# Kernel tuning notes

Hardware: AMD Instinct MI355X
Metric: run time of the kernel (lower is better)

The kernel has to match this reference:

```python
import jax, jax.numpy as jnp
import numpy as np

B, T, C = 2, 2048, 2048
N_HEAD = 16
HS = C // N_HEAD
D_LATENT = C // 2


def setup_inputs() -> dict:
    key = jax.random.key(0)
    ks = jax.random.split(key, 7)
    s = 0.02
    return {
        "x": jax.random.normal(ks[0], (B, T, C), dtype=jnp.float32),
        "Wq": jax.random.normal(ks[1], (C, C), dtype=jnp.float32) * s,
        "Wc": jax.random.normal(ks[2], (C, D_LATENT), dtype=jnp.float32) * s,
        "Wk": jax.random.normal(ks[3], (D_LATENT, C), dtype=jnp.float32) * s,
        "Wv": jax.random.normal(ks[4], (D_LATENT, C), dtype=jnp.float32) * s,
        "Wo": jax.random.normal(ks[5], (C, C), dtype=jnp.float32) * s,
        "bo": jnp.zeros((C,), dtype=jnp.float32),
    }


def reference(x, Wq, Wc, Wk, Wv, Wo, bo):
    b, t, c = x.shape
    # projections (torch Linear without bias, weights stored as (in, out))
    q = x @ Wq                    # (B,T,C)
    c_latent = x @ Wc             # (B,T,d_latent)
    k = c_latent @ Wk             # (B,T,C)
    v = c_latent @ Wv             # (B,T,C)
    # split heads -> (B,H,T,hs)
    q = q.reshape(b, t, N_HEAD, HS).transpose(0, 2, 1, 3)
    k = k.reshape(b, t, N_HEAD, HS).transpose(0, 2, 1, 3)
    v = v.reshape(b, t, N_HEAD, HS).transpose(0, 2, 1, 3)
    scale = 1.0 / jnp.sqrt(jnp.asarray(HS, dtype=x.dtype))
    scores = jnp.einsum('bhqd,bhkd->bhqk', q, k) * scale
    causal = jnp.tril(jnp.ones((t, t), dtype=bool))
    scores = jnp.where(causal, scores, jnp.finfo(scores.dtype).min)
    attn = jax.nn.softmax(scores, axis=-1)
    y = jnp.einsum('bhqk,bhkd->bhqd', attn, v)      # (B,H,T,hs)
    y = y.transpose(0, 2, 1, 3).reshape(b, t, c)
    return y @ Wo + bo
```

## Files before the change

### kernel.cpp

```cpp
#include <hip/hip_runtime.h>
#include <hip/hip_bf16.h>
#include <math.h>

typedef __hip_bfloat16 bf16;
typedef __attribute__((ext_vector_type(8))) short bf16x8;
typedef __attribute__((ext_vector_type(4))) float f32x4;

#define B_  2
#define T_  2048
#define C_  2048
#define H_  16
#define HS_ 128
#define DL_ 1024
#define M_  (B_ * T_)
#define NT64_ 32

__device__ inline void lds16(const bf16* g, bf16* l) {
    __builtin_amdgcn_global_load_lds(
        (const __attribute__((address_space(1))) void*)g,
        (__attribute__((address_space(3))) void*)l, 16, 0, 0);
}

__global__ __launch_bounds__(256) void cast_bf16_k(
    const float* __restrict__ in, bf16* __restrict__ out)
{
    const size_t i = ((size_t)blockIdx.x * 256 + threadIdx.x) * 8;
    const float4 a = *(const float4*)(in + i);
    const float4 b = *(const float4*)(in + i + 4);
    bf16 o[8];
    o[0] = __float2bfloat16(a.x); o[1] = __float2bfloat16(a.y);
    o[2] = __float2bfloat16(a.z); o[3] = __float2bfloat16(a.w);
    o[4] = __float2bfloat16(b.x); o[5] = __float2bfloat16(b.y);
    o[6] = __float2bfloat16(b.z); o[7] = __float2bfloat16(b.w);
    *(uint4*)(out + i) = *(const uint4*)o;
}

__global__ __launch_bounds__(256) void transpose_cast5(
    const float* __restrict__ s0, const float* __restrict__ s1,
    const float* __restrict__ s2, const float* __restrict__ s3,
    const float* __restrict__ s4,
    bf16* __restrict__ d0, bf16* __restrict__ d1, bf16* __restrict__ d2,
    bf16* __restrict__ d3, bf16* __restrict__ d4)
{
    const float* in; bf16* out; int R, Cc;
    switch (blockIdx.z) {
        case 0: in = s0; out = d0; R = C_;  Cc = C_;  break;
        case 1: in = s1; out = d1; R = C_;  Cc = DL_; break;
        case 2: in = s2; out = d2; R = DL_; Cc = C_;  break;
        case 3: in = s3; out = d3; R = DL_; Cc = C_;  break;
        default: in = s4; out = d4; R = C_; Cc = C_;  break;
    }
    const int bx = blockIdx.x * 32, by = blockIdx.y * 32;
    if (bx >= Cc || by >= R) return;
    __shared__ float t[32][33];
    const int tx = threadIdx.x & 31, ty = threadIdx.x >> 5;
#pragma unroll
    for (int i = 0; i < 32; i += 8)
        t[ty + i][tx] = in[(size_t)(by + ty + i) * Cc + bx + tx];
    __syncthreads();
#pragma unroll
    for (int i = 0; i < 32; i += 8)
        out[(size_t)(bx + ty + i) * R + by + tx] = __float2bfloat16(t[tx][ty + i]);
}

#define GEMM250_CORE(A_, Bt_, ldA_, ldB_, Kdim_)                               \
    __shared__ __align__(16) bf16 smem[3 * 24576];                 \
    const int tid  = threadIdx.x;                                              \
    const int lane = tid & 63;                                                 \
    const int wid  = tid >> 6;                                       \
    const int wr   = wid >> 1, wc = wid & 1;                    \
    const int quad = lane >> 4, l16 = lane & 15;                               \
    const int sw8  = (l16 >> 1) & 7;                                           \
    f32x4 acc[4][4];                                                           \
    _Pragma("unroll")                                                          \
    for (int i = 0; i < 4; i++)                                                \
        _Pragma("unroll")                                                      \
        for (int j = 0; j < 4; j++) acc[i][j] = (f32x4){0.f, 0.f, 0.f, 0.f};   \
    const int sr  = tid >> 3;                                       \
    const int ssl = ((tid & 7) ^ ((sr >> 1) & 7)) * 8;                         \
    const bf16* pa = (A_)  + (size_t)(m0 + sr) * (ldA_) + ssl;                 \
    const bf16* pb = (Bt_) + (size_t)(n0 + sr) * (ldB_) + ssl;                 \
    const size_t a64 = (size_t)64 * (ldA_), b64 = (size_t)64 * (ldB_);         \
    const int NT = (Kdim_) / 64;                                               \
    _Pragma("unroll")                                                          \
    for (int pt = 0; pt < 2; ++pt) {                  \
        bf16* dst = smem + pt * 24576 + tid * 8;                               \
        const size_t ko = (size_t)pt * 64;                                     \
        lds16(pa + ko,           dst);                                         \
        lds16(pa + a64 + ko,     dst + 4096);                                  \
        lds16(pa + 2*a64 + ko,   dst + 8192);                                  \
        lds16(pa + 3*a64 + ko,   dst + 12288);                                 \
        lds16(pb + ko,           dst + 16384);                                 \
        lds16(pb + b64 + ko,     dst + 20480);                                 \
    }                                                                          \
    int cur = 0, nxt2 = 2;                                                     \
    for (int t = 0; t < NT; ++t) {                                             \
        if (t == NT - 1) {                                                     \
            __asm__ __volatile__("s_waitcnt vmcnt(0)" ::: "memory");           \
        } else {                                                               \
            __asm__ __volatile__("s_waitcnt vmcnt(6)" ::: "memory");           \
        }                                                                      \
        __builtin_amdgcn_s_barrier();                                          \
        __builtin_amdgcn_sched_barrier(0);                                     \
        if (t + 2 < NT) {                                                      \
            bf16* dst = smem + nxt2 * 24576 + tid * 8;                         \
            const size_t ko = (size_t)(t + 2) * 64;                            \
            lds16(pa + ko,           dst);                                     \
            lds16(pa + a64 + ko,     dst + 4096);                              \
            lds16(pa + 2*a64 + ko,   dst + 8192);                              \
            lds16(pa + 3*a64 + ko,   dst + 12288);                             \
            lds16(pb + ko,           dst + 16384);                             \
            lds16(pb + b64 + ko,     dst + 20480);                             \
        }                                                                      \
        const bf16* Ab = smem + cur * 24576;                                   \
        const bf16* Bb = Ab + 16384;                                           \
        bf16x8 af[4][2], bfr[4][2];                                            \
        _Pragma("unroll")                                                      \
        for (int mi = 0; mi < 4; mi++)                                         \
            _Pragma("unroll")                                                  \
            for (int ks = 0; ks < 2; ks++)                                     \
                af[mi][ks] = *(const bf16x8*)&Ab[(wr*64 + mi*16 + l16)*64 +    \
                                                 (((ks<<2)|quad) ^ sw8)*8];    \
        _Pragma("unroll")                                                      \
        for (int ni = 0; ni < 4; ni++)                                         \
            _Pragma("unroll")                                                  \
            for (int ks = 0; ks < 2; ks++)                                     \
                bfr[ni][ks] = *(const bf16x8*)&Bb[(wc*64 + ni*16 + l16)*64 +   \
                                                  (((ks<<2)|quad) ^ sw8)*8];   \
        __builtin_amdgcn_s_setprio(1);                                         \
        _Pragma("unroll")                                                      \
        for (int ks = 0; ks < 2; ks++)                                         \
            _Pragma("unroll")                                                  \
            for (int mi = 0; mi < 4; mi++)                                     \
                _Pragma("unroll")                                              \
                for (int ni = 0; ni < 4; ni++)                                 \
                    acc[mi][ni] = __builtin_amdgcn_mfma_f32_16x16x32_bf16(     \
                        af[mi][ks], bfr[ni][ks], acc[mi][ni], 0, 0, 0);        \
        __builtin_amdgcn_s_setprio(0);                                         \
        cur  = (cur  == 2) ? 0 : cur  + 1;                                     \
        nxt2 = (nxt2 == 2) ? 0 : nxt2 + 1;                                     \
    }

__global__ __launch_bounds__(512, 2) void gemm_qc_250(
    const bf16* __restrict__ A, const bf16* __restrict__ Bt,
    bf16* __restrict__ Cq, bf16* __restrict__ Cc)
{
    const int m0 = blockIdx.y * 256, n0 = blockIdx.x * 128;
    GEMM250_CORE(A, Bt, C_, C_, C_)
    const bool is_q = (n0 < C_);
    const float scl = is_q ? 0.08838834764831845f : 1.0f;
    bf16* dst = is_q ? Cq : Cc;
    const int ld   = is_q ? C_ : DL_;
    const int coff = is_q ? 0 : C_;
#pragma unroll
    for (int mi = 0; mi < 4; mi++) {
#pragma unroll
        for (int ni = 0; ni < 4; ni++) {
            const int col = n0 - coff + wc * 64 + ni * 16 + l16;
#pragma unroll
            for (int r = 0; r < 4; r++) {
                const int row = m0 + wr * 64 + mi * 16 + quad * 4 + r;
                dst[(size_t)row * ld + col] = __float2bfloat16(acc[mi][ni][r] * scl);
            }
        }
    }
}

__global__ __launch_bounds__(512, 2) void gemm_kv_250(
    const bf16* __restrict__ clat, const bf16* __restrict__ Wk_t,
    const bf16* __restrict__ Wv_t, bf16* __restrict__ kk, bf16* __restrict__ vt)
{
    const int bid = blockIdx.x;
    const bf16 *A, *Bt; bf16* dst; int N, m0, n0;
    if (bid < 256) { A = clat; Bt = Wk_t; dst = kk; N = C_;
                     m0 = (bid >> 4) * 256; n0 = (bid & 15) * 128; }
    else           { const int t2 = bid - 256;
                     A = Wv_t; Bt = clat; dst = vt; N = M_;
                     m0 = (t2 >> 5) * 256; n0 = (t2 & 31) * 128; }
    GEMM250_CORE(A, Bt, DL_, DL_, DL_)
#pragma unroll
    for (int mi = 0; mi < 4; mi++) {
#pragma unroll
        for (int ni = 0; ni < 4; ni++) {
            const int col = n0 + wc * 64 + ni * 16 + l16;
#pragma unroll
            for (int r = 0; r < 4; r++) {
                const int row = m0 + wr * 64 + mi * 16 + quad * 4 + r;
                dst[(size_t)row * N + col] = __float2bfloat16(acc[mi][ni][r]);
            }
        }
    }
}

__global__ __launch_bounds__(512, 2) void gemm_out_250(
    const bf16* __restrict__ A, const bf16* __restrict__ Bt,
    float* __restrict__ Cf32, const float* __restrict__ bias)
{
    const int m0 = blockIdx.y * 256, n0 = blockIdx.x * 128;
    GEMM250_CORE(A, Bt, C_, C_, C_)
#pragma unroll
    for (int mi = 0; mi < 4; mi++) {
#pragma unroll
        for (int ni = 0; ni < 4; ni++) {
            const int col = n0 + wc * 64 + ni * 16 + l16;
#pragma unroll
            for (int r = 0; r < 4; r++) {
                const int row = m0 + wr * 64 + mi * 16 + quad * 4 + r;
                Cf32[(size_t)row * C_ + col] = acc[mi][ni][r] + bias[col];
            }
        }
    }
}

__global__ __launch_bounds__(256, 2) void flash_dual(
    const bf16* __restrict__ Q, const bf16* __restrict__ K,
    const bf16* __restrict__ Vt, bf16* __restrict__ Y)
{
    __shared__ __align__(16) bf16 Ks[2][4][64][32];
    __shared__ __align__(16) bf16 Vs[2][2][128][32];
    __shared__ __align__(16) bf16 Ps[4][16][72];
    const int tid  = threadIdx.x;
    const int lane = tid & 63, wv = tid >> 6;
    const int quad = lane >> 4, l16 = lane & 15;
    const int sw = (l16 >> 1) & 3;
    const int bid = blockIdx.x;
    const int bh = (bid & 7) * 4 + ((bid >> 3) & 3);
    const int pa = bid >> 5;
    const int b = bh >> 4, h = bh & 15;
    const int qA0 = pa * 64, qB0 = (NT64_ - 1 - pa) * 64;
    const int jA = pa + 1;
    const int jB = NT64_ - pa;

    const int sr  = tid >> 2;
    const int ssl = ((tid & 3) ^ ((sr >> 1) & 3)) * 8;

    bf16x8 qfA[4], qfB[4];
    {
        const size_t rA = (size_t)(b * T_ + qA0 + wv * 16 + l16) * C_ + h * HS_;
        const size_t rB = (size_t)(b * T_ + qB0 + wv * 16 + l16) * C_ + h * HS_;
#pragma unroll
        for (int c = 0; c < 4; c++) {
            qfA[c] = *(const bf16x8*)(Q + rA + c * 32 + quad * 8);
            qfB[c] = *(const bf16x8*)(Q + rB + c * 32 + quad * 8);
        }
    }

    f32x4 oA[8], oB[8];
#pragma unroll
    for (int dt = 0; dt < 8; dt++) {
        oA[dt] = (f32x4){0.f, 0.f, 0.f, 0.f};
        oB[dt] = (f32x4){0.f, 0.f, 0.f, 0.f};
    }
    float lA[4] = {0.f, 0.f, 0.f, 0.f}, lB[4] = {0.f, 0.f, 0.f, 0.f};
    const int rbA = qA0 + wv * 16, rbB = qB0 + wv * 16;

    auto stage = [&](int j, int sbuf) {
        const int kv0 = j * 64;
#pragma unroll
        for (int kc = 0; kc < 4; kc++)
            lds16(K + (size_t)(b * T_ + kv0 + sr) * C_ + h * HS_ + kc * 32 + ssl,
                  &Ks[sbuf][kc][0][0] + tid * 8);
#pragma unroll
        for (int vc = 0; vc < 2; vc++)
#pragma unroll
            for (int hf = 0; hf < 2; hf++)
                lds16(Vt + (size_t)(h * HS_ + hf * 64 + sr) * M_ + b * T_ + kv0 + vc * 32 + ssl,
                      &Vs[sbuf][vc][hf * 64][0] + tid * 8);
    };

    auto sm_half = [&](const f32x4* s, int nt0, float* l_s, bool diag,
                       int kv0, int rowbase) {
        float p[2][4];
#pragma unroll
        for (int t = 0; t < 2; t++)
#pragma unroll
            for (int r = 0; r < 4; r++) {
                const int nt = nt0 + t;
                float e = __expf(s[nt][r]);
                if (diag) {
                    const int col = kv0 + nt * 16 + l16;
                    const int row = rowbase + quad * 4 + r;
                    if (col > row) e = 0.f;
                }
                p[t][r] = e;
            }
#pragma unroll
        for (int r = 0; r < 4; r++) l_s[r] += p[0][r] + p[1][r];
#pragma unroll
        for (int t = 0; t < 2; t++)
#pragma unroll
            for (int r = 0; r < 4; r++)
                Ps[wv][quad * 4 + r][(nt0 + t) * 16 + l16] = __float2bfloat16(p[t][r]);
        return *(const bf16x8*)&Ps[wv][l16][nt0 * 16 + quad * 8];
    };

    stage(0, 0);

    for (int j = 0; j < jA; j++) {
        const int kv0 = j * 64;
        stage(j + 1, (j + 1) & 1);
        __asm__ __volatile__("s_waitcnt vmcnt(8)" ::: "memory");
        __builtin_amdgcn_s_barrier();
        const int buf = j & 1;

        f32x4 sA[4], sB[4];
#pragma unroll
        for (int nt = 0; nt < 4; nt++) {
            sA[nt] = (f32x4){0.f, 0.f, 0.f, 0.f};
            sB[nt] = (f32x4){0.f, 0.f, 0.f, 0.f};
        }
        __builtin_amdgcn_s_setprio(1);
#pragma unroll
        for (int c = 0; c < 4; c++) {
            bf16x8 kf[4];
#pragma unroll
            for (int nt = 0; nt < 4; nt++)
                kf[nt] = *(const bf16x8*)&Ks[buf][c][nt * 16 + l16][(quad ^ sw) * 8];
#pragma unroll
            for (int nt = 0; nt < 4; nt++) {
                sB[nt] = __builtin_amdgcn_mfma_f32_16x16x32_bf16(qfB[c], kf[nt], sB[nt], 0, 0, 0);
                sA[nt] = __builtin_amdgcn_mfma_f32_16x16x32_bf16(qfA[c], kf[nt], sA[nt], 0, 0, 0);
            }
        }
        __builtin_amdgcn_s_setprio(0);

        const bool dA = (j == jA - 1);
        const bf16x8 pB0 = sm_half(sB, 0, lB, false, kv0, rbB);
        const bf16x8 pB1 = sm_half(sB, 2, lB, false, kv0, rbB);
        const bf16x8 pA0 = sm_half(sA, 0, lA, dA, kv0, rbA);
        const bf16x8 pA1 = sm_half(sA, 2, lA, dA, kv0, rbA);

        __builtin_amdgcn_s_setprio(1);
#pragma unroll
        for (int dt = 0; dt < 8; dt++) {
            const bf16x8 vf0 = *(const bf16x8*)&Vs[buf][0][dt * 16 + l16][(quad ^ sw) * 8];
            oB[dt] = __builtin_amdgcn_mfma_f32_16x16x32_bf16(pB0, vf0, oB[dt], 0, 0, 0);
            oA[dt] = __builtin_amdgcn_mfma_f32_16x16x32_bf16(pA0, vf0, oA[dt], 0, 0, 0);
        }
#pragma unroll
        for (int dt = 0; dt < 8; dt++) {
            const bf16x8 vf1 = *(const bf16x8*)&Vs[buf][1][dt * 16 + l16][(quad ^ sw) * 8];
            oB[dt] = __builtin_amdgcn_mfma_f32_16x16x32_bf16(pB1, vf1, oB[dt], 0, 0, 0);
            oA[dt] = __builtin_amdgcn_mfma_f32_16x16x32_bf16(pA1, vf1, oA[dt], 0, 0, 0);
        }
        __builtin_amdgcn_s_setprio(0);
        __asm__ __volatile__("s_waitcnt lgkmcnt(0)" ::: "memory");
        __builtin_amdgcn_s_barrier();
    }

    for (int j = jA; j < jB; j++) {
        const int kv0 = j * 64;
        if (j + 1 < jB) {
            stage(j + 1, (j + 1) & 1);
            __asm__ __volatile__("s_waitcnt vmcnt(8)" ::: "memory");
        } else {
            __asm__ __volatile__("s_waitcnt vmcnt(0)" ::: "memory");
        }
        __builtin_amdgcn_s_barrier();
        const int buf = j & 1;

        f32x4 sB[4];
#pragma unroll
        for (int nt = 0; nt < 4; nt++) sB[nt] = (f32x4){0.f, 0.f, 0.f, 0.f};
        __builtin_amdgcn_s_setprio(1);
#pragma unroll
        for (int c = 0; c < 4; c++) {
            bf16x8 kf[4];
#pragma unroll
            for (int nt = 0; nt < 4; nt++)
                kf[nt] = *(const bf16x8*)&Ks[buf][c][nt * 16 + l16][(quad ^ sw) * 8];
#pragma unroll
            for (int nt = 0; nt < 4; nt++)
                sB[nt] = __builtin_amdgcn_mfma_f32_16x16x32_bf16(qfB[c], kf[nt], sB[nt], 0, 0, 0);
        }
        __builtin_amdgcn_s_setprio(0);

        const bool dB = (j == jB - 1);
        const bf16x8 pB0 = sm_half(sB, 0, lB, dB, kv0, rbB);
        const bf16x8 pB1 = sm_half(sB, 2, lB, dB, kv0, rbB);

        __builtin_amdgcn_s_setprio(1);
#pragma unroll
        for (int dt = 0; dt < 8; dt++) {
            const bf16x8 vf0 = *(const bf16x8*)&Vs[buf][0][dt * 16 + l16][(quad ^ sw) * 8];
            oB[dt] = __builtin_amdgcn_mfma_f32_16x16x32_bf16(pB0, vf0, oB[dt], 0, 0, 0);
        }
#pragma unroll
        for (int dt = 0; dt < 8; dt++) {
            const bf16x8 vf1 = *(const bf16x8*)&Vs[buf][1][dt * 16 + l16][(quad ^ sw) * 8];
            oB[dt] = __builtin_amdgcn_mfma_f32_16x16x32_bf16(pB1, vf1, oB[dt], 0, 0, 0);
        }
        __builtin_amdgcn_s_setprio(0);
        __asm__ __volatile__("s_waitcnt lgkmcnt(0)" ::: "memory");
        __builtin_amdgcn_s_barrier();
    }

    auto finish = [&](int q0, f32x4* oacc, float* l_s) {
        float inv[4];
#pragma unroll
        for (int r = 0; r < 4; r++) {
            float l = l_s[r];
            l += __shfl_xor(l, 1);
            l += __shfl_xor(l, 2);
            l += __shfl_xor(l, 4);
            l += __shfl_xor(l, 8);
            inv[r] = 1.f / l;
        }
        const int rowbase = q0 + wv * 16;
#pragma unroll
        for (int dt = 0; dt < 8; dt++)
#pragma unroll
            for (int r = 0; r < 4; r++)
                Y[(size_t)(b * T_ + rowbase + quad * 4 + r) * C_ + h * HS_ + dt * 16 + l16] =
                    __float2bfloat16(oacc[dt][r] * inv[r]);
    };
    finish(qA0, oA, lA);
    finish(qB0, oB, lB);
}

extern "C" void kernel_launch(void* const* d_in, const int* in_sizes, int n_in,
                              void* d_out, int out_size, void* d_ws, size_t ws_size,
                              hipStream_t stream) {
    const float* x  = (const float*)d_in[0];
    const float* Wq = (const float*)d_in[1];
    const float* Wc = (const float*)d_in[2];
    const float* Wk = (const float*)d_in[3];
    const float* Wv = (const float*)d_in[4];
    const float* Wo = (const float*)d_in[5];
    const float* bo = (const float*)d_in[6];
    float* out = (float*)d_out;

    bf16* ws   = (bf16*)d_ws;
    bf16* x_bf = ws;
    bf16* Wq_t = x_bf + (size_t)M_ * C_;
    bf16* Wc_t = Wq_t + (size_t)C_ * C_;
    bf16* Wk_t = Wc_t + (size_t)DL_ * C_;
    bf16* Wv_t = Wk_t + (size_t)C_ * DL_;
    bf16* Wo_t = Wv_t + (size_t)C_ * DL_;
    bf16* q    = Wo_t + (size_t)C_ * C_;
    bf16* clat = q    + (size_t)M_ * C_;
    bf16* kk   = clat + (size_t)M_ * DL_;
    bf16* vt   = kk   + (size_t)M_ * C_;
    bf16* y    = vt   + (size_t)C_ * M_;

    const dim3 blk(256);
    const dim3 blk512(512);

    cast_bf16_k<<<dim3((M_ * C_) / (256 * 8)), blk, 0, stream>>>(x, x_bf);
    transpose_cast5<<<dim3(C_ / 32, C_ / 32, 5), blk, 0, stream>>>(
        Wq, Wc, Wk, Wv, Wo, Wq_t, Wc_t, Wk_t, Wv_t, Wo_t);

    gemm_qc_250<<<dim3((C_ + DL_) / 128, M_ / 256), blk512, 0, stream>>>(
        x_bf, Wq_t, q, clat);
    gemm_kv_250<<<dim3(512), blk512, 0, stream>>>(clat, Wk_t, Wv_t, kk, vt);

    flash_dual<<<dim3((NT64_ / 2) * H_ * B_), blk, 0, stream>>>(q, kk, vt, y);

    gemm_out_250<<<dim3(C_ / 128, M_ / 256), blk512, 0, stream>>>(
        y, Wo_t, out, bo);
}
```

Measured before the change: 333.3 us.

## Split GEMM K-halves across waves with LDS reduction and XCD-aware tile mapping

```diff
diff --git a/kernel.cpp b/kernel.cpp
--- a/kernel.cpp
+++ b/kernel.cpp
@@ -68,12 +68,14 @@
     const int tid  = threadIdx.x;                                              \
     const int lane = tid & 63;                                                 \
     const int wid  = tid >> 6;                                       \
-    const int wr   = wid >> 1, wc = wid & 1;                    \
+    const int kh   = wid & 1;                                      \
+    const int wc   = (wid >> 1) & 1;                           \
+    const int wr   = wid >> 2;                                 \
     const int quad = lane >> 4, l16 = lane & 15;                               \
     const int sw8  = (l16 >> 1) & 7;                                           \
-    f32x4 acc[4][4];                                                           \
+    f32x4 acc[8][4];                                                           \
     _Pragma("unroll")                                                          \
-    for (int i = 0; i < 4; i++)                                                \
+    for (int i = 0; i < 8; i++)                                                \
         _Pragma("unroll")                                                      \
         for (int j = 0; j < 4; j++) acc[i][j] = (f32x4){0.f, 0.f, 0.f, 0.f};   \
     const int sr  = tid >> 3;                                       \
@@ -114,53 +116,72 @@
         }                                                                      \
         const bf16* Ab = smem + cur * 24576;                                   \
         const bf16* Bb = Ab + 16384;                                           \
-        bf16x8 af[4][2], bfr[4][2];                                            \
+        bf16x8 af[8], bfr[4];                                                  \
         _Pragma("unroll")                                                      \
-        for (int mi = 0; mi < 4; mi++)                                         \
-            _Pragma("unroll")                                                  \
-            for (int ks = 0; ks < 2; ks++)                                     \
-                af[mi][ks] = *(const bf16x8*)&Ab[(wr*64 + mi*16 + l16)*64 +    \
-                                                 (((ks<<2)|quad) ^ sw8)*8];    \
+        for (int mi = 0; mi < 8; mi++)                                         \
+            af[mi] = *(const bf16x8*)&Ab[(wr*128 + mi*16 + l16)*64 +           \
+                                         (((kh<<2)|quad) ^ sw8)*8];            \
         _Pragma("unroll")                                                      \
         for (int ni = 0; ni < 4; ni++)                                         \
-            _Pragma("unroll")                                                  \
-            for (int ks = 0; ks < 2; ks++)                                     \
-                bfr[ni][ks] = *(const bf16x8*)&Bb[(wc*64 + ni*16 + l16)*64 +   \
-                                                  (((ks<<2)|quad) ^ sw8)*8];   \
+            bfr[ni] = *(const bf16x8*)&Bb[(wc*64 + ni*16 + l16)*64 +           \
+                                          (((kh<<2)|quad) ^ sw8)*8];           \
         __builtin_amdgcn_s_setprio(1);                                         \
         _Pragma("unroll")                                                      \
-        for (int ks = 0; ks < 2; ks++)                                         \
+        for (int mi = 0; mi < 8; mi++)                                         \
             _Pragma("unroll")                                                  \
-            for (int mi = 0; mi < 4; mi++)                                     \
-                _Pragma("unroll")                                              \
-                for (int ni = 0; ni < 4; ni++)                                 \
-                    acc[mi][ni] = __builtin_amdgcn_mfma_f32_16x16x32_bf16(     \
-                        af[mi][ks], bfr[ni][ks], acc[mi][ni], 0, 0, 0);        \
+            for (int ni = 0; ni < 4; ni++)                                     \
+                acc[mi][ni] = __builtin_amdgcn_mfma_f32_16x16x32_bf16(         \
+                    af[mi], bfr[ni], acc[mi][ni], 0, 0, 0);                    \
         __builtin_amdgcn_s_setprio(0);                                         \
         cur  = (cur  == 2) ? 0 : cur  + 1;                                     \
         nxt2 = (nxt2 == 2) ? 0 : nxt2 + 1;                                     \
+    }                                                                          \
+    __syncthreads();                              \
+    {                                                                          \
+        float* red = (float*)smem + (size_t)((wr << 1) | wc) * 8192;           \
+        if (kh) {                                                              \
+            _Pragma("unroll")                                                  \
+            for (int mi = 0; mi < 8; mi++)                                     \
+                _Pragma("unroll")                                              \
+                for (int ni = 0; ni < 4; ni++)                                 \
+                    *(f32x4*)(red + (mi*4 + ni)*256 + lane*4) = acc[mi][ni];   \
+        }                                                                      \
+    }                                                                          \
+    __syncthreads();                                                           \
+    if (!kh) {                                                                 \
+        const float* red = (const float*)smem + (size_t)((wr << 1) | wc) * 8192;\
+        _Pragma("unroll")                                                      \
+        for (int mi = 0; mi < 8; mi++)                                         \
+            _Pragma("unroll")                                                  \
+            for (int ni = 0; ni < 4; ni++)                                     \
+                acc[mi][ni] += *(const f32x4*)(red + (mi*4 + ni)*256 + lane*4);\
     }
 
 __global__ __launch_bounds__(512, 2) void gemm_qc_250(
     const bf16* __restrict__ A, const bf16* __restrict__ Bt,
     bf16* __restrict__ Cq, bf16* __restrict__ Cc)
 {
-    const int m0 = blockIdx.y * 256, n0 = blockIdx.x * 128;
+    const int lin = blockIdx.y * 24 + blockIdx.x;
+    const int xcd = lin & 7, ii = lin >> 3;
+    const int m0 = (ii & 15) * 256;
+    const int n0 = (xcd * 3 + (ii >> 4)) * 128;
     GEMM250_CORE(A, Bt, C_, C_, C_)
-    const bool is_q = (n0 < C_);
-    const float scl = is_q ? 0.08838834764831845f : 1.0f;
-    bf16* dst = is_q ? Cq : Cc;
-    const int ld   = is_q ? C_ : DL_;
-    const int coff = is_q ? 0 : C_;
-#pragma unroll
-    for (int mi = 0; mi < 4; mi++) {
-#pragma unroll
-        for (int ni = 0; ni < 4; ni++) {
-            const int col = n0 - coff + wc * 64 + ni * 16 + l16;
-#pragma unroll
-            for (int r = 0; r < 4; r++) {
-                const int row = m0 + wr * 64 + mi * 16 + quad * 4 + r;
-                dst[(size_t)row * ld + col] = __float2bfloat16(acc[mi][ni][r] * scl);
+    if (!kh) {
+        const bool is_q = (n0 < C_);
+        const float scl = is_q ? 0.08838834764831845f : 1.0f;
+        bf16* dst = is_q ? Cq : Cc;
+        const int ld   = is_q ? C_ : DL_;
+        const int coff = is_q ? 0 : C_;
+#pragma unroll
+        for (int mi = 0; mi < 8; mi++) {
+#pragma unroll
+            for (int ni = 0; ni < 4; ni++) {
+                const int col = n0 - coff + wc * 64 + ni * 16 + l16;
+#pragma unroll
+                for (int r = 0; r < 4; r++) {
+                    const int row = m0 + wr * 128 + mi * 16 + quad * 4 + r;
+                    dst[(size_t)row * ld + col] = __float2bfloat16(acc[mi][ni][r] * scl);
+                }
             }
         }
     }
@@ -172,21 +193,30 @@
 {
     const int bid = blockIdx.x;
     const bf16 *A, *Bt; bf16* dst; int N, m0, n0;
-    if (bid < 256) { A = clat; Bt = Wk_t; dst = kk; N = C_;
-                     m0 = (bid >> 4) * 256; n0 = (bid & 15) * 128; }
-    else           { const int t2 = bid - 256;
-                     A = Wv_t; Bt = clat; dst = vt; N = M_;
-                     m0 = (t2 >> 5) * 256; n0 = (t2 & 31) * 128; }
+    if (bid < 256) {
+        const int xcd = bid & 7, ii = bid >> 3;
+        A = clat; Bt = Wk_t; dst = kk; N = C_;
+        m0 = (ii & 15) * 256;
+        n0 = (xcd * 2 + (ii >> 4)) * 128;
+    } else {
+        const int t2 = bid - 256;
+        const int xcd = t2 & 7, ii = t2 >> 3;
+        A = Wv_t; Bt = clat; dst = vt; N = M_;
+        m0 = (ii & 7) * 256;
+        n0 = (xcd * 4 + (ii >> 3)) * 128;
+    }
     GEMM250_CORE(A, Bt, DL_, DL_, DL_)
-#pragma unroll
-    for (int mi = 0; mi < 4; mi++) {
-#pragma unroll
-        for (int ni = 0; ni < 4; ni++) {
-            const int col = n0 + wc * 64 + ni * 16 + l16;
-#pragma unroll
-            for (int r = 0; r < 4; r++) {
-                const int row = m0 + wr * 64 + mi * 16 + quad * 4 + r;
-                dst[(size_t)row * N + col] = __float2bfloat16(acc[mi][ni][r]);
+    if (!kh) {
+#pragma unroll
+        for (int mi = 0; mi < 8; mi++) {
+#pragma unroll
+            for (int ni = 0; ni < 4; ni++) {
+                const int col = n0 + wc * 64 + ni * 16 + l16;
+#pragma unroll
+                for (int r = 0; r < 4; r++) {
+                    const int row = m0 + wr * 128 + mi * 16 + quad * 4 + r;
+                    dst[(size_t)row * N + col] = __float2bfloat16(acc[mi][ni][r]);
+                }
             }
         }
     }
@@ -196,17 +226,22 @@
     const bf16* __restrict__ A, const bf16* __restrict__ Bt,
     float* __restrict__ Cf32, const float* __restrict__ bias)
 {
-    const int m0 = blockIdx.y * 256, n0 = blockIdx.x * 128;
+    const int lin = blockIdx.y * 16 + blockIdx.x;
+    const int xcd = lin & 7, ii = lin >> 3;
+    const int m0 = (ii & 15) * 256;
+    const int n0 = (xcd * 2 + (ii >> 4)) * 128;
     GEMM250_CORE(A, Bt, C_, C_, C_)
-#pragma unroll
-    for (int mi = 0; mi < 4; mi++) {
-#pragma unroll
-        for (int ni = 0; ni < 4; ni++) {
-            const int col = n0 + wc * 64 + ni * 16 + l16;
-#pragma unroll
-            for (int r = 0; r < 4; r++) {
-                const int row = m0 + wr * 64 + mi * 16 + quad * 4 + r;
-                Cf32[(size_t)row * C_ + col] = acc[mi][ni][r] + bias[col];
+    if (!kh) {
+#pragma unroll
+        for (int mi = 0; mi < 8; mi++) {
+#pragma unroll
+            for (int ni = 0; ni < 4; ni++) {
+                const int col = n0 + wc * 64 + ni * 16 + l16;
+#pragma unroll
+                for (int r = 0; r < 4; r++) {
+                    const int row = m0 + wr * 128 + mi * 16 + quad * 4 + r;
+                    Cf32[(size_t)row * C_ + col] = acc[mi][ni][r] + bias[col];
+                }
             }
         }
     }
```

New measurement: 361.7 us. 8.5% more time.

## Replace dual-tile flash kernel with single-tile kernel loading V from global

Applied to the files above, without the earlier changes.

```diff
diff --git a/kernel.cpp b/kernel.cpp
--- a/kernel.cpp
+++ b/kernel.cpp
@@ -212,12 +212,11 @@
     }
 }
 
-__global__ __launch_bounds__(256, 2) void flash_dual(
+__global__ __launch_bounds__(256, 3) void flash_v(
     const bf16* __restrict__ Q, const bf16* __restrict__ K,
     const bf16* __restrict__ Vt, bf16* __restrict__ Y)
 {
     __shared__ __align__(16) bf16 Ks[2][4][64][32];
-    __shared__ __align__(16) bf16 Vs[2][2][128][32];
     __shared__ __align__(16) bf16 Ps[4][16][72];
     const int tid  = threadIdx.x;
     const int lane = tid & 63, wv = tid >> 6;
@@ -225,51 +224,38 @@
     const int sw = (l16 >> 1) & 3;
     const int bid = blockIdx.x;
     const int bh = (bid & 7) * 4 + ((bid >> 3) & 3);
-    const int pa = bid >> 5;
+    const int pa = (NT64_ - 1) - (bid >> 5);
     const int b = bh >> 4, h = bh & 15;
-    const int qA0 = pa * 64, qB0 = (NT64_ - 1 - pa) * 64;
-    const int jA = pa + 1;
-    const int jB = NT64_ - pa;
+    const int q0 = pa * 64;
+    const int nj = pa + 1;
+    const int rb = q0 + wv * 16;
 
     const int sr  = tid >> 2;
     const int ssl = ((tid & 3) ^ ((sr >> 1) & 3)) * 8;
 
-    bf16x8 qfA[4], qfB[4];
+    bf16x8 qf[4];
     {
-        const size_t rA = (size_t)(b * T_ + qA0 + wv * 16 + l16) * C_ + h * HS_;
-        const size_t rB = (size_t)(b * T_ + qB0 + wv * 16 + l16) * C_ + h * HS_;
-#pragma unroll
-        for (int c = 0; c < 4; c++) {
-            qfA[c] = *(const bf16x8*)(Q + rA + c * 32 + quad * 8);
-            qfB[c] = *(const bf16x8*)(Q + rB + c * 32 + quad * 8);
-        }
-    }
-
-    f32x4 oA[8], oB[8];
-#pragma unroll
-    for (int dt = 0; dt < 8; dt++) {
-        oA[dt] = (f32x4){0.f, 0.f, 0.f, 0.f};
-        oB[dt] = (f32x4){0.f, 0.f, 0.f, 0.f};
-    }
-    float lA[4] = {0.f, 0.f, 0.f, 0.f}, lB[4] = {0.f, 0.f, 0.f, 0.f};
-    const int rbA = qA0 + wv * 16, rbB = qB0 + wv * 16;
-
-    auto stage = [&](int j, int sbuf) {
+        const size_t rQ = (size_t)(b * T_ + q0 + wv * 16 + l16) * C_ + h * HS_;
+#pragma unroll
+        for (int c = 0; c < 4; c++)
+            qf[c] = *(const bf16x8*)(Q + rQ + c * 32 + quad * 8);
+    }
+    const bf16* vrow = Vt + (size_t)(h * HS_ + l16) * M_ + b * T_ + quad * 8;
+
+    f32x4 o[8];
+#pragma unroll
+    for (int dt = 0; dt < 8; dt++) o[dt] = (f32x4){0.f, 0.f, 0.f, 0.f};
+    float l_s[4] = {0.f, 0.f, 0.f, 0.f};
+
+    auto stageK = [&](int j, int sbuf) {
         const int kv0 = j * 64;
 #pragma unroll
         for (int kc = 0; kc < 4; kc++)
             lds16(K + (size_t)(b * T_ + kv0 + sr) * C_ + h * HS_ + kc * 32 + ssl,
                   &Ks[sbuf][kc][0][0] + tid * 8);
-#pragma unroll
-        for (int vc = 0; vc < 2; vc++)
-#pragma unroll
-            for (int hf = 0; hf < 2; hf++)
-                lds16(Vt + (size_t)(h * HS_ + hf * 64 + sr) * M_ + b * T_ + kv0 + vc * 32 + ssl,
-                      &Vs[sbuf][vc][hf * 64][0] + tid * 8);
     };
 
-    auto sm_half = [&](const f32x4* s, int nt0, float* l_s, bool diag,
-                       int kv0, int rowbase) {
+    auto sm_half = [&](const f32x4* s, int nt0, bool diag, int kv0) {
         float p[2][4];
 #pragma unroll
         for (int t = 0; t < 2; t++)
@@ -279,7 +265,7 @@
                 float e = __expf(s[nt][r]);
                 if (diag) {
                     const int col = kv0 + nt * 16 + l16;
-                    const int row = rowbase + quad * 4 + r;
+                    const int row = rb + quad * 4 + r;
                     if (col > row) e = 0.f;
                 }
                 p[t][r] = e;
@@ -294,21 +280,21 @@
         return *(const bf16x8*)&Ps[wv][l16][nt0 * 16 + quad * 8];
     };
 
-    stage(0, 0);
-
-    for (int j = 0; j < jA; j++) {
+    stageK(0, 0);
+    for (int j = 0; j < nj; j++) {
         const int kv0 = j * 64;
-        stage(j + 1, (j + 1) & 1);
-        __asm__ __volatile__("s_waitcnt vmcnt(8)" ::: "memory");
+        if (j + 1 < nj) {
+            stageK(j + 1, (j + 1) & 1);
+            __asm__ __volatile__("s_waitcnt vmcnt(4)" ::: "memory");
+        } else {
+            __asm__ __volatile__("s_waitcnt vmcnt(0)" ::: "memory");
+        }
         __builtin_amdgcn_s_barrier();
         const int buf = j & 1;
 
-        f32x4 sA[4], sB[4];
-#pragma unroll
-        for (int nt = 0; nt < 4; nt++) {
-            sA[nt] = (f32x4){0.f, 0.f, 0.f, 0.f};
-            sB[nt] = (f32x4){0.f, 0.f, 0.f, 0.f};
-        }
+        f32x4 s[4];
+#pragma unroll
+        for (int nt = 0; nt < 4; nt++) s[nt] = (f32x4){0.f, 0.f, 0.f, 0.f};
         __builtin_amdgcn_s_setprio(1);
 #pragma unroll
         for (int c = 0; c < 4; c++) {
@@ -317,85 +303,32 @@
             for (int nt = 0; nt < 4; nt++)
                 kf[nt] = *(const bf16x8*)&Ks[buf][c][nt * 16 + l16][(quad ^ sw) * 8];
 #pragma unroll
-            for (int nt = 0; nt < 4; nt++) {
-                sB[nt] = __builtin_amdgcn_mfma_f32_16x16x32_bf16(qfB[c], kf[nt], sB[nt], 0, 0, 0);
-                sA[nt] = __builtin_amdgcn_mfma_f32_16x16x32_bf16(qfA[c], kf[nt], sA[nt], 0, 0, 0);
-            }
+            for (int nt = 0; nt < 4; nt++)
+                s[nt] = __builtin_amdgcn_mfma_f32_16x16x32_bf16(qf[c], kf[nt], s[nt], 0, 0, 0);
         }
         __builtin_amdgcn_s_setprio(0);
 
-        const bool dA = (j == jA - 1);
-        const bf16x8 pB0 = sm_half(sB, 0, lB, false, kv0, rbB);
-        const bf16x8 pB1 = sm_half(sB, 2, lB, false, kv0, rbB);
-        const bf16x8 pA0 = sm_half(sA, 0, lA, dA, kv0, rbA);
-        const bf16x8 pA1 = sm_half(sA, 2, lA, dA, kv0, rbA);
+        const bool dg = (j == nj - 1);
+        const bf16x8 p0 = sm_half(s, 0, dg, kv0);
+        const bf16x8 p1 = sm_half(s, 2, dg, kv0);
 
         __builtin_amdgcn_s_setprio(1);
 #pragma unroll
         for (int dt = 0; dt < 8; dt++) {
-            const bf16x8 vf0 = *(const bf16x8*)&Vs[buf][0][dt * 16 + l16][(quad ^ sw) * 8];
-            oB[dt] = __builtin_amdgcn_mfma_f32_16x16x32_bf16(pB0, vf0, oB[dt], 0, 0, 0);
-            oA[dt] = __builtin_amdgcn_mfma_f32_16x16x32_bf16(pA0, vf0, oA[dt], 0, 0, 0);
+            const bf16x8 vf0 = *(const bf16x8*)(vrow + (size_t)(dt * 16) * M_ + kv0);
+            o[dt] = __builtin_amdgcn_mfma_f32_16x16x32_bf16(p0, vf0, o[dt], 0, 0, 0);
         }
 #pragma unroll
         for (int dt = 0; dt < 8; dt++) {
-            const bf16x8 vf1 = *(const bf16x8*)&Vs[buf][1][dt * 16 + l16][(quad ^ sw) * 8];
-            oB[dt] = __builtin_amdgcn_mfma_f32_16x16x32_bf16(pB1, vf1, oB[dt], 0, 0, 0);
-            oA[dt] = __builtin_amdgcn_mfma_f32_16x16x32_bf16(pA1, vf1, oA[dt], 0, 0, 0);
+            const bf16x8 vf1 = *(const bf16x8*)(vrow + (size_t)(dt * 16) * M_ + kv0 + 32);
+            o[dt] = __builtin_amdgcn_mfma_f32_16x16x32_bf16(p1, vf1, o[dt], 0, 0, 0);
         }
         __builtin_amdgcn_s_setprio(0);
         __asm__ __volatile__("s_waitcnt lgkmcnt(0)" ::: "memory");
         __builtin_amdgcn_s_barrier();
     }
 
-    for (int j = jA; j < jB; j++) {
-        const int kv0 = j * 64;
-        if (j + 1 < jB) {
-            stage(j + 1, (j + 1) & 1);
-            __asm__ __volatile__("s_waitcnt vmcnt(8)" ::: "memory");
-        } else {
-            __asm__ __volatile__("s_waitcnt vmcnt(0)" ::: "memory");
-        }
-        __builtin_amdgcn_s_barrier();
-        const int buf = j & 1;
-
-        f32x4 sB[4];
-#pragma unroll
-        for (int nt = 0; nt < 4; nt++) sB[nt] = (f32x4){0.f, 0.f, 0.f, 0.f};
-        __builtin_amdgcn_s_setprio(1);
-#pragma unroll
-        for (int c = 0; c < 4; c++) {
-            bf16x8 kf[4];
-#pragma unroll
-            for (int nt = 0; nt < 4; nt++)
-                kf[nt] = *(const bf16x8*)&Ks[buf][c][nt * 16 + l16][(quad ^ sw) * 8];
-#pragma unroll
-            for (int nt = 0; nt < 4; nt++)
-                sB[nt] = __builtin_amdgcn_mfma_f32_16x16x32_bf16(qfB[c], kf[nt], sB[nt], 0, 0, 0);
-        }
-        __builtin_amdgcn_s_setprio(0);
-
-        const bool dB = (j == jB - 1);
-        const bf16x8 pB0 = sm_half(sB, 0, lB, dB, kv0, rbB);
-        const bf16x8 pB1 = sm_half(sB, 2, lB, dB, kv0, rbB);
-
-        __builtin_amdgcn_s_setprio(1);
-#pragma unroll
-        for (int dt = 0; dt < 8; dt++) {
-            const bf16x8 vf0 = *(const bf16x8*)&Vs[buf][0][dt * 16 + l16][(quad ^ sw) * 8];
-            oB[dt] = __builtin_amdgcn_mfma_f32_16x16x32_bf16(pB0, vf0, oB[dt], 0, 0, 0);
-        }
-#pragma unroll
-        for (int dt = 0; dt < 8; dt++) {
-            const bf16x8 vf1 = *(const bf16x8*)&Vs[buf][1][dt * 16 + l16][(quad ^ sw) * 8];
-            oB[dt] = __builtin_amdgcn_mfma_f32_16x16x32_bf16(pB1, vf1, oB[dt], 0, 0, 0);
-        }
-        __builtin_amdgcn_s_setprio(0);
-        __asm__ __volatile__("s_waitcnt lgkmcnt(0)" ::: "memory");
-        __builtin_amdgcn_s_barrier();
-    }
-
-    auto finish = [&](int q0, f32x4* oacc, float* l_s) {
+    {
         float inv[4];
 #pragma unroll
         for (int r = 0; r < 4; r++) {
@@ -406,16 +339,13 @@
             l += __shfl_xor(l, 8);
             inv[r] = 1.f / l;
         }
-        const int rowbase = q0 + wv * 16;
 #pragma unroll
         for (int dt = 0; dt < 8; dt++)
 #pragma unroll
             for (int r = 0; r < 4; r++)
-                Y[(size_t)(b * T_ + rowbase + quad * 4 + r) * C_ + h * HS_ + dt * 16 + l16] =
-                    __float2bfloat16(oacc[dt][r] * inv[r]);
-    };
-    finish(qA0, oA, lA);
-    finish(qB0, oB, lB);
+                Y[(size_t)(b * T_ + rb + quad * 4 + r) * C_ + h * HS_ + dt * 16 + l16] =
+                    __float2bfloat16(o[dt][r] * inv[r]);
+    }
 }
 
 extern "C" void kernel_launch(void* const* d_in, const int* in_sizes, int n_in,
@@ -454,7 +384,7 @@
         x_bf, Wq_t, q, clat);
     gemm_kv_250<<<dim3(512), blk512, 0, stream>>>(clat, Wk_t, Wv_t, kk, vt);
 
-    flash_dual<<<dim3((NT64_ / 2) * H_ * B_), blk, 0, stream>>>(q, kk, vt, y);
+    flash_v<<<dim3(NT64_ * H_ * B_), blk, 0, stream>>>(q, kk, vt, y);
 
     gemm_out_250<<<dim3(C_ / 128, M_ / 256), blk512, 0, stream>>>(
         y, Wo_t, out, bo);
```

New measurement: 442.4 us. +32.7%, slower.
